# Kernel tuning notes

Hardware: AMD Instinct MI355X
Metric: run time of the kernel (lower is better)

Reference implementation:

```python
import jax, jax.numpy as jnp
import numpy as np

T, B, I, H = 512, 64, 1024, 1024
G = 4 * H + 1  # 4 LSTM gates + 1 boundary gate (HM-LSTM)
STDV = 1.0 / np.sqrt(H)


def setup_inputs() -> dict:
    key = jax.random.key(0)
    ks = jax.random.split(key, 5)
    u = lambda k, shape: jax.random.uniform(k, shape, jnp.float32, -STDV, STDV)
    return {
        "x": jax.random.normal(ks[0], (T, B, I), jnp.float32),
        "W_ih": u(ks[1], (G, I)),
        "W_hh": u(ks[2], (G, H)),
        "b_ih": u(ks[3], (G,)),
        "b_hh": u(ks[4], (G,)),
    }


def reference(x, W_ih, W_hh, b_ih, b_hh):
    h_dim = W_hh.shape[1]
    # Precompute input contribution for all timesteps in one big GEMM: [T,B,G]
    gx_all = jnp.einsum("tbi,gi->tbg", x, W_ih) + b_ih + b_hh
    Bsz = x.shape[1]
    h0 = jnp.zeros((Bsz, h_dim), x.dtype)
    c0 = jnp.zeros((Bsz, h_dim), x.dtype)

    def step(carry, gx):
        h, c = carry
        g = gx + h @ W_hh.T  # [B, 4H+1]
        i = jax.nn.sigmoid(g[:, :h_dim])
        f = jax.nn.sigmoid(g[:, h_dim:2 * h_dim])
        gg = jnp.tanh(g[:, 2 * h_dim:3 * h_dim])
        o = jax.nn.sigmoid(g[:, 3 * h_dim:4 * h_dim])
        z = jax.nn.sigmoid(g[:, 4 * h_dim:])  # [B,1] boundary gate
        ig = i * gg
        # HM-LSTM soft boundary: FLUSH (c=i*g) when z->1, UPDATE otherwise
        c_new = z * ig + (1.0 - z) * (f * c + ig)
        h_new = o * jnp.tanh(c_new)
        return (h_new, c_new), h_new

    (hT, cT), out = jax.lax.scan(step, (h0, c0), gx_all)
    return out, hT, cT
```

## Files before the change

### kernel.cpp

```cpp
#include <hip/hip_runtime.h>
#include <cstdint>
#include <cstddef>

typedef unsigned short u16;
typedef short bf16x8 __attribute__((ext_vector_type(8)));
typedef u16   u16x8  __attribute__((ext_vector_type(8)));
typedef float f32x4  __attribute__((ext_vector_type(4)));

#define NT  512
#define NB  64
#define NH  1024
#define NTB 32768
#define G4  4096

#define AS1C(p) ((const __attribute__((address_space(1))) void*)(p))
#define AS3(p)  ((__attribute__((address_space(3))) void*)(p))

__device__ __forceinline__ float b2f(u16 u){
  return __uint_as_float(((unsigned)u) << 16);
}
__device__ __forceinline__ u16 f2b(float f){
  unsigned u = __float_as_uint(f);
  return (u16)((u + 0x7fffu + ((u >> 16) & 1u)) >> 16);
}
__device__ __forceinline__ float fsigmoid(float x){
  return __builtin_amdgcn_rcpf(1.f + __builtin_amdgcn_exp2f(-1.442695041f * x));
}
__device__ __forceinline__ float ftanh(float x){
  return 2.f * __builtin_amdgcn_rcpf(1.f + __builtin_amdgcn_exp2f(-2.885390082f * x)) - 1.f;
}

__global__ void cvt_bf16(const float* __restrict__ in, u16* __restrict__ out, int n8){
  int stride = gridDim.x * blockDim.x;
  for (int i = blockIdx.x * blockDim.x + threadIdx.x; i < n8; i += stride){
    const float4* p = (const float4*)(in + (size_t)i * 8);
    float4 a = p[0], b = p[1];
    u16x8 r;
    r[0]=f2b(a.x); r[1]=f2b(a.y); r[2]=f2b(a.z); r[3]=f2b(a.w);
    r[4]=f2b(b.x); r[5]=f2b(b.y); r[6]=f2b(b.z); r[7]=f2b(b.w);
    *(u16x8*)(out + (size_t)i * 8) = r;
  }
}

__global__ void zpre_kernel(const float* __restrict__ x, const float* __restrict__ Wih,
                            const float* __restrict__ b_ih, const float* __restrict__ b_hh,
                            float* __restrict__ zp){
  int gw   = (blockIdx.x * 256 + threadIdx.x) >> 6;
  int lane = threadIdx.x & 63;
  const float* wz = Wih + (size_t)4096 * 1024;
  float4 wv[4];
  #pragma unroll
  for (int j = 0; j < 4; ++j) wv[j] = *(const float4*)&wz[lane*16 + j*4];
  float bz = b_ih[4096] + b_hh[4096];
  for (int r = gw; r < NTB; r += 1024){
    const float* xr = x + (size_t)r * 1024 + lane * 16;
    float s = 0.f;
    #pragma unroll
    for (int j = 0; j < 4; ++j){
      float4 xv = *(const float4*)&xr[j*4];
      s += xv.x*wv[j].x + xv.y*wv[j].y + xv.z*wv[j].z + xv.w*wv[j].w;
    }
    #pragma unroll
    for (int o = 32; o > 0; o >>= 1) s += __shfl_down(s, o);
    if (lane == 0) zp[r] = s + bz;
  }
}

template<typename GT>
__global__ __launch_bounds__(256, 2) void gemm_gx(
    const u16* __restrict__ Xb, const u16* __restrict__ Wb,
    const float* __restrict__ b_ih, const float* __restrict__ b_hh,
    GT* __restrict__ gx)
{
  __shared__ u16 As[128*32];
  __shared__ u16 Bs[128*32];
  const int tid  = threadIdx.x;
  const int lane = tid & 63, wave = tid >> 6;
  const int wr = wave >> 1, wc = wave & 1;
  const int m0 = (blockIdx.x & 255) * 128;
  const int n0 = (blockIdx.x >> 8) * 128;
  const int srow = wave * 16 + (lane >> 2);
  const int scol = (lane & 3) * 8;
  const u16* gA = Xb + (size_t)(m0 + srow) * 1024 + scol;
  const u16* gB = Wb + (size_t)(n0 + srow) * 1024 + scol;
  char* lA = (char*)As + wave * 1024;
  char* lB = (char*)Bs + wave * 1024;
  const int fr = lane & 15, fo = (lane >> 4) * 8;

  f32x4 acc[4][4] = {};
  for (int k0 = 0; k0 < 1024; k0 += 32){
    __syncthreads();
    __builtin_amdgcn_global_load_lds(AS1C(gA + k0),            AS3(lA),        16, 0, 0);
    __builtin_amdgcn_global_load_lds(AS1C(gA + 64*1024 + k0),  AS3(lA + 4096), 16, 0, 0);
    __builtin_amdgcn_global_load_lds(AS1C(gB + k0),            AS3(lB),        16, 0, 0);
    __builtin_amdgcn_global_load_lds(AS1C(gB + 64*1024 + k0),  AS3(lB + 4096), 16, 0, 0);
    __syncthreads();
    bf16x8 a[4], b[4];
    #pragma unroll
    for (int mi = 0; mi < 4; ++mi)
      a[mi] = *(const bf16x8*)&As[(wr*64 + mi*16 + fr)*32 + fo];
    #pragma unroll
    for (int ni = 0; ni < 4; ++ni)
      b[ni] = *(const bf16x8*)&Bs[(wc*64 + ni*16 + fr)*32 + fo];
    #pragma unroll
    for (int mi = 0; mi < 4; ++mi)
      #pragma unroll
      for (int ni = 0; ni < 4; ++ni)
        acc[mi][ni] = __builtin_amdgcn_mfma_f32_16x16x32_bf16(a[mi], b[ni], acc[mi][ni], 0, 0, 0);
  }
  const int orow = (lane >> 4) * 4, ocol = lane & 15;
  #pragma unroll
  for (int ni = 0; ni < 4; ++ni){
    const int g = n0 + wc*64 + ni*16 + ocol;
    const float bias = b_ih[g] + b_hh[g];
    #pragma unroll
    for (int mi = 0; mi < 4; ++mi){
      const size_t rb = (size_t)(m0 + wr*64 + mi*16 + orow);
      #pragma unroll
      for (int r = 0; r < 4; ++r){
        float v = acc[mi][ni][r] + bias;
        if constexpr (sizeof(GT) == 4)
          __builtin_nontemporal_store(v, (float*)gx + (rb + r)*G4 + g);
        else
          __builtin_nontemporal_store(f2b(v), (u16*)gx + (rb + r)*G4 + g);
      }
    }
  }
}

__device__ __forceinline__ uint4 ld_h(const uint4* p, bool fb){
  uint4 r;
  if (fb) asm volatile("global_load_dwordx4 %0, %1, off sc0 sc1" : "=v"(r) : "v"(p) : "memory");
  else    asm volatile("global_load_dwordx4 %0, %1, off sc0"     : "=v"(r) : "v"(p) : "memory");
  return r;
}

template<typename GT>
__global__ __launch_bounds__(512, 2) void hmlstm_scan(
    const u16* __restrict__ Whhb, const float* __restrict__ Whhf,
    const GT* __restrict__ gx, const float* __restrict__ zpre,
    unsigned* __restrict__ hdw, float* __restrict__ out)
{
  const int tid  = threadIdx.x;
  const int lane = tid & 63, wave = tid >> 6;
  const int gw = wave >> 1, cb = wave & 1;
  const int fr = lane & 15, hi4 = lane >> 4;
  const int g  = blockIdx.x & 7;
  const int hb = blockIdx.x >> 3;

  __shared__ u16   hs[8*1024];
  __shared__ float wzf[1024];
  __shared__ float glds[4][8][32];
  __shared__ float zsum[8];

  for (int i = tid; i < 1024; i += 512) wzf[i] = Whhf[(size_t)4096*1024 + i];

  const int grow = gw*1024 + hb*32 + cb*16 + fr;
  bf16x8 Bw[32];
  #pragma unroll
  for (int kc = 0; kc < 32; ++kc)
    Bw[kc] = *(const bf16x8*)&Whhb[(size_t)grow*1024 + kc*32 + hi4*8];
  #pragma unroll
  for (int kc = 0; kc < 32; ++kc)
    asm volatile("" : "+v"(Bw[kc]));

  if (tid < 256){
    int b = tid >> 5, c = tid & 31;
    unsigned* p = hdw + (size_t)(g*8 + b)*1024 + hb*32 + c;
    unsigned v0 = 1u;
    asm volatile("global_store_dword %0, %1, off sc0 sc1" :: "v"(p), "v"(v0) : "memory");
  }

  const int srow = wave;
  const int scol = (lane) * 16;
  float c_reg = 0.f;
  bool  fb = false;

  for (int t = 0; t < NT; ++t){
    const unsigned* src = hdw + (size_t)(t & 1) * 65536;
    unsigned*       dst = hdw + (size_t)((t + 1) & 1) * 65536;
    const unsigned  tgt = (unsigned)(t + 1);
    const unsigned* rbase = src + (size_t)(g*8 + srow)*1024 + scol;

    uint4 v[4];
    #pragma unroll
    for (int q = 0; q < 4; ++q) v[q] = ld_h((const uint4*)(rbase + q*4), fb);

    float gxl[4]; float zpc;
    {
      const GT* gp = gx + ((size_t)t*64 + g*8 + (hi4 & 1)*4)*G4 + grow;
      if constexpr (sizeof(GT) == 4){
        #pragma unroll
        for (int r = 0; r < 4; ++r)
          asm volatile("global_load_dword %0, %1, off nt" : "=v"(gxl[r]) : "v"((const float*)gp + (size_t)r*G4) : "memory");
      } else {
        #pragma unroll
        for (int r = 0; r < 4; ++r)
          asm volatile("global_load_ushort %0, %1, off nt" : "=v"(*(unsigned*)&gxl[r]) : "v"((const u16*)gp + (size_t)r*G4) : "memory");
      }
      asm volatile("global_load_dword %0, %1, off" : "=v"(zpc) : "v"(zpre + t*64 + g*8 + ((tid>>5)&7)) : "memory");
    }
    asm volatile("s_waitcnt vmcnt(5)" ::: "memory");
    __builtin_amdgcn_sched_barrier(0);

    unsigned pend = 0;
    #pragma unroll
    for (int q = 0; q < 4; ++q){
      unsigned m = ((v[q].x^tgt)|(v[q].y^tgt)|(v[q].z^tgt)|(v[q].w^tgt)) & 0xFFFFu;
      pend |= (m == 0) ? 0u : (1u << q);
    }
    int spin = 0;
    while (__any((int)(pend != 0u))){
      if (++spin > 8){ fb = true; }
      fb = (bool)__any((int)fb);
      #pragma unroll
      for (int q = 0; q < 4; ++q)
        if (__any((int)((pend >> q) & 1u)))
          v[q] = ld_h((const uint4*)(rbase + q*4), fb);
      asm volatile("s_waitcnt vmcnt(0)" ::: "memory");
      __builtin_amdgcn_sched_barrier(0);
      #pragma unroll
      for (int q = 0; q < 4; ++q){
        if ((pend >> q) & 1u){
          unsigned m = ((v[q].x^tgt)|(v[q].y^tgt)|(v[q].z^tgt)|(v[q].w^tgt)) & 0xFFFFu;
          if (m == 0) pend &= ~(1u << q);
        }
      }
    }

    #pragma unroll
    for (int q = 0; q < 4; ++q){
      unsigned p0 = (v[q].x >> 16) | (v[q].y & 0xFFFF0000u);
      unsigned p1 = (v[q].z >> 16) | (v[q].w & 0xFFFF0000u);
      uint2 pw = {p0, p1};
      int u16b = lane*32 + (q >> 1)*16;
      int addr = srow*2048 + ((u16b ^ (srow << 4))) + (q & 1)*8;
      *(uint2*)((char*)hs + addr) = pw;
    }
    __syncthreads();

    f32x4 acc0 = {}, acc1 = {}, acc2 = {}, acc3 = {};
    const int arow = fr & 7;
    #pragma unroll
    for (int kc = 0; kc < 32; kc += 4){
      bf16x8 a0 = *(const bf16x8*)((char*)hs + arow*2048 + (((kc+0)*64 + hi4*16) ^ (arow << 4)));
      bf16x8 a1 = *(const bf16x8*)((char*)hs + arow*2048 + (((kc+1)*64 + hi4*16) ^ (arow << 4)));
      bf16x8 a2 = *(const bf16x8*)((char*)hs + arow*2048 + (((kc+2)*64 + hi4*16) ^ (arow << 4)));
      bf16x8 a3 = *(const bf16x8*)((char*)hs + arow*2048 + (((kc+3)*64 + hi4*16) ^ (arow << 4)));
      acc0 = __builtin_amdgcn_mfma_f32_16x16x32_bf16(a0, Bw[kc+0], acc0, 0, 0, 0);
      acc1 = __builtin_amdgcn_mfma_f32_16x16x32_bf16(a1, Bw[kc+1], acc1, 0, 0, 0);
      acc2 = __builtin_amdgcn_mfma_f32_16x16x32_bf16(a2, Bw[kc+2], acc2, 0, 0, 0);
      acc3 = __builtin_amdgcn_mfma_f32_16x16x32_bf16(a3, Bw[kc+3], acc3, 0, 0, 0);
    }
    f32x4 ac = (acc0 + acc1) + (acc2 + acc3);

    {
      int bz = wave;
      float zp = 0.f;
      int b0 = bz*2048 + ((lane*32) ^ (bz << 4));
      int b1 = bz*2048 + ((lane*32 + 16) ^ (bz << 4));
      bf16x8 h0 = *(const bf16x8*)((char*)hs + b0);
      bf16x8 h1 = *(const bf16x8*)((char*)hs + b1);
      #pragma unroll
      for (int e = 0; e < 8; ++e){
        zp += b2f((u16)h0[e]) * wzf[lane*16 + e];
        zp += b2f((u16)h1[e]) * wzf[lane*16 + 8 + e];
      }
      #pragma unroll
      for (int o = 32; o > 0; o >>= 1) zp += __shfl_xor(zp, o);
      if (lane == 0) zsum[bz] = zp;
    }

    asm volatile("s_waitcnt vmcnt(0)" ::: "memory");
    __builtin_amdgcn_sched_barrier(0);

    if constexpr (sizeof(GT) != 4){
      #pragma unroll
      for (int r = 0; r < 4; ++r)
        gxl[r] = __uint_as_float((*(unsigned*)&gxl[r]) << 16);
    }

    if (hi4 < 2){
      #pragma unroll
      for (int r = 0; r < 4; ++r){
        float vv = ac[r] + gxl[r];
        float s = (gw == 2) ? ftanh(vv) : fsigmoid(vv);
        glds[gw][hi4*4 + r][cb*16 + fr] = s;
      }
    }
    __syncthreads();

    if (tid < 256){
      int b = tid >> 5, c = tid & 31;
      float iv  = glds[0][b][c], fvg = glds[1][b][c];
      float gv  = glds[2][b][c], ov  = glds[3][b][c];
      float zv  = fsigmoid(zpc + zsum[b]);
      float ig  = iv * gv;
      float cn  = zv*ig + (1.f - zv)*(fvg*c_reg + ig);
      float hv_ = ov * ftanh(cn);
      c_reg = cn;
      const int hoff = (g*8 + b)*1024 + hb*32 + c;
      unsigned pv = ((unsigned)f2b(hv_) << 16) | (unsigned)(t + 2);
      asm volatile("global_store_dword %0, %1, off sc0 sc1" :: "v"(dst + hoff), "v"(pv) : "memory");
      __builtin_nontemporal_store(hv_, out + (size_t)t*65536 + hoff);
      if (t == NT-1){
        out[(size_t)NT*65536 + hoff] = hv_;
        out[(size_t)NT*65536 + 65536 + hoff] = cn;
      }
    }
  }
}

extern "C" void kernel_launch(void* const* d_in, const int* in_sizes, int n_in,
                              void* d_out, int out_size, void* d_ws, size_t ws_size,
                              hipStream_t stream)
{
  (void)in_sizes; (void)n_in; (void)out_size;
  const float* x    = (const float*)d_in[0];
  const float* Wih  = (const float*)d_in[1];
  const float* Whh  = (const float*)d_in[2];
  const float* b_ih = (const float*)d_in[3];
  const float* b_hh = (const float*)d_in[4];
  float* out = (float*)d_out;

  size_t off = 0;
  auto alloc = [&](size_t bytes)->void*{
    void* p = (char*)d_ws + off;
    off = (off + bytes + 255) & ~(size_t)255;
    return p;
  };
  u16*  xb    = (u16*) alloc((size_t)NTB*1024*2);
  u16*  wihb  = (u16*) alloc((size_t)4097*1024*2);
  u16*  whhb  = (u16*) alloc((size_t)4097*1024*2);
  unsigned* hdw = (unsigned*)alloc((size_t)2*65536*4);
  float* zp   = (float*)alloc((size_t)NTB*4);
  bool g32 = (ws_size >= off + (size_t)NTB*G4*4);
  void* gxp = (char*)d_ws + off;

  hipMemsetAsync(hdw, 0, (size_t)2*65536*4, stream);
  cvt_bf16<<<dim3(2048), dim3(256), 0, stream>>>(x,   xb,   NTB*1024/8);
  cvt_bf16<<<dim3(512),  dim3(256), 0, stream>>>(Wih, wihb, 4097*1024/8);
  cvt_bf16<<<dim3(512),  dim3(256), 0, stream>>>(Whh, whhb, 4097*1024/8);
  zpre_kernel<<<dim3(256), dim3(256), 0, stream>>>(x, Wih, b_ih, b_hh, zp);
  if (g32){
    float* gxf = (float*)gxp;
    gemm_gx<float><<<dim3(8192), dim3(256), 0, stream>>>(xb, wihb, b_ih, b_hh, gxf);
    void* args[] = { (void*)&whhb, (void*)&Whh, (void*)&gxf, (void*)&zp, (void*)&hdw, (void*)&out };
    if (hipLaunchCooperativeKernel((void*)hmlstm_scan<float>, dim3(256), dim3(512),
                                   args, 0, stream) != hipSuccess)
      hmlstm_scan<float><<<dim3(256), dim3(512), 0, stream>>>(whhb, Whh, gxf, zp, hdw, out);
  } else {
    u16* gxb = (u16*)gxp;
    gemm_gx<u16><<<dim3(8192), dim3(256), 0, stream>>>(xb, wihb, b_ih, b_hh, gxb);
    void* args[] = { (void*)&whhb, (void*)&Whh, (void*)&gxb, (void*)&zp, (void*)&hdw, (void*)&out };
    if (hipLaunchCooperativeKernel((void*)hmlstm_scan<u16>, dim3(256), dim3(512),
                                   args, 0, stream) != hipSuccess)
      hmlstm_scan<u16><<<dim3(256), dim3(512), 0, stream>>>(whhb, Whh, gxb, zp, hdw, out);
  }
}
```

Before: 3.577 ms.

## Keep W_hh fragments in AGPRs and fuse boundary-gate dot into h unpack

```diff
diff --git a/kernel.cpp b/kernel.cpp
--- a/kernel.cpp
+++ b/kernel.cpp
@@ -137,9 +137,9 @@
 
 template<typename GT>
 __global__ __launch_bounds__(512, 2) void hmlstm_scan(
-    const u16* __restrict__ Whhb, const float* __restrict__ Whhf,
-    const GT* __restrict__ gx, const float* __restrict__ zpre,
-    unsigned* __restrict__ hdw, float* __restrict__ out)
+    const u16* __restrict__ Whhb, const GT* __restrict__ gx,
+    const float* __restrict__ zpre, unsigned* __restrict__ hdw,
+    float* __restrict__ out)
 {
   const int tid  = threadIdx.x;
   const int lane = tid & 63, wave = tid >> 6;
@@ -149,12 +149,9 @@
   const int hb = blockIdx.x >> 3;
 
   __shared__ u16   hs[8*1024];
-  __shared__ float wzf[1024];
   __shared__ float glds[4][8][32];
   __shared__ float zsum[8];
 
-  for (int i = tid; i < 1024; i += 512) wzf[i] = Whhf[(size_t)4096*1024 + i];
-
   const int grow = gw*1024 + hb*32 + cb*16 + fr;
   bf16x8 Bw[32];
   #pragma unroll
@@ -162,7 +159,12 @@
     Bw[kc] = *(const bf16x8*)&Whhb[(size_t)grow*1024 + kc*32 + hi4*8];
   #pragma unroll
   for (int kc = 0; kc < 32; ++kc)
-    asm volatile("" : "+v"(Bw[kc]));
+    asm volatile("" : "+a"(Bw[kc]));
+
+  uint2 wzr[4];
+  #pragma unroll
+  for (int q = 0; q < 4; ++q)
+    wzr[q] = *(const uint2*)&Whhb[(size_t)4096*1024 + lane*16 + q*4];
 
   if (tid < 256){
     int b = tid >> 5, c = tid & 31;
@@ -172,7 +174,7 @@
   }
 
   const int srow = wave;
-  const int scol = (lane) * 16;
+  const int scol = lane * 16;
   float c_reg = 0.f;
   bool  fb = false;
 
@@ -228,15 +230,23 @@
       }
     }
 
+    float zp = 0.f;
     #pragma unroll
     for (int q = 0; q < 4; ++q){
       unsigned p0 = (v[q].x >> 16) | (v[q].y & 0xFFFF0000u);
       unsigned p1 = (v[q].z >> 16) | (v[q].w & 0xFFFF0000u);
+      zp = fmaf(__uint_as_float(p0 << 16),         __uint_as_float(wzr[q].x << 16),         zp);
+      zp = fmaf(__uint_as_float(p0 & 0xFFFF0000u), __uint_as_float(wzr[q].x & 0xFFFF0000u), zp);
+      zp = fmaf(__uint_as_float(p1 << 16),         __uint_as_float(wzr[q].y << 16),         zp);
+      zp = fmaf(__uint_as_float(p1 & 0xFFFF0000u), __uint_as_float(wzr[q].y & 0xFFFF0000u), zp);
       uint2 pw = {p0, p1};
       int u16b = lane*32 + (q >> 1)*16;
       int addr = srow*2048 + ((u16b ^ (srow << 4))) + (q & 1)*8;
       *(uint2*)((char*)hs + addr) = pw;
     }
+    #pragma unroll
+    for (int o = 32; o > 0; o >>= 1) zp += __shfl_xor(zp, o);
+    if (lane == 0) zsum[srow] = zp;
     __syncthreads();
 
     f32x4 acc0 = {}, acc1 = {}, acc2 = {}, acc3 = {};
@@ -247,29 +257,13 @@
       bf16x8 a1 = *(const bf16x8*)((char*)hs + arow*2048 + (((kc+1)*64 + hi4*16) ^ (arow << 4)));
       bf16x8 a2 = *(const bf16x8*)((char*)hs + arow*2048 + (((kc+2)*64 + hi4*16) ^ (arow << 4)));
       bf16x8 a3 = *(const bf16x8*)((char*)hs + arow*2048 + (((kc+3)*64 + hi4*16) ^ (arow << 4)));
-      acc0 = __builtin_amdgcn_mfma_f32_16x16x32_bf16(a0, Bw[kc+0], acc0, 0, 0, 0);
-      acc1 = __builtin_amdgcn_mfma_f32_16x16x32_bf16(a1, Bw[kc+1], acc1, 0, 0, 0);
-      acc2 = __builtin_amdgcn_mfma_f32_16x16x32_bf16(a2, Bw[kc+2], acc2, 0, 0, 0);
-      acc3 = __builtin_amdgcn_mfma_f32_16x16x32_bf16(a3, Bw[kc+3], acc3, 0, 0, 0);
-    }
+      asm volatile("v_mfma_f32_16x16x32_bf16 %0, %1, %2, %0" : "+v"(acc0) : "v"(a0), "a"(Bw[kc+0]));
+      asm volatile("v_mfma_f32_16x16x32_bf16 %0, %1, %2, %0" : "+v"(acc1) : "v"(a1), "a"(Bw[kc+1]));
+      asm volatile("v_mfma_f32_16x16x32_bf16 %0, %1, %2, %0" : "+v"(acc2) : "v"(a2), "a"(Bw[kc+2]));
+      asm volatile("v_mfma_f32_16x16x32_bf16 %0, %1, %2, %0" : "+v"(acc3) : "v"(a3), "a"(Bw[kc+3]));
+    }
+    asm volatile("s_nop 7\n\ts_nop 7\n\ts_nop 7" :::);
     f32x4 ac = (acc0 + acc1) + (acc2 + acc3);
-
-    {
-      int bz = wave;
-      float zp = 0.f;
-      int b0 = bz*2048 + ((lane*32) ^ (bz << 4));
-      int b1 = bz*2048 + ((lane*32 + 16) ^ (bz << 4));
-      bf16x8 h0 = *(const bf16x8*)((char*)hs + b0);
-      bf16x8 h1 = *(const bf16x8*)((char*)hs + b1);
-      #pragma unroll
-      for (int e = 0; e < 8; ++e){
-        zp += b2f((u16)h0[e]) * wzf[lane*16 + e];
-        zp += b2f((u16)h1[e]) * wzf[lane*16 + 8 + e];
-      }
-      #pragma unroll
-      for (int o = 32; o > 0; o >>= 1) zp += __shfl_xor(zp, o);
-      if (lane == 0) zsum[bz] = zp;
-    }
 
     asm volatile("s_waitcnt vmcnt(0)" ::: "memory");
     __builtin_amdgcn_sched_barrier(0);
@@ -345,16 +339,16 @@
   if (g32){
     float* gxf = (float*)gxp;
     gemm_gx<float><<<dim3(8192), dim3(256), 0, stream>>>(xb, wihb, b_ih, b_hh, gxf);
-    void* args[] = { (void*)&whhb, (void*)&Whh, (void*)&gxf, (void*)&zp, (void*)&hdw, (void*)&out };
+    void* args[] = { (void*)&whhb, (void*)&gxf, (void*)&zp, (void*)&hdw, (void*)&out };
     if (hipLaunchCooperativeKernel((void*)hmlstm_scan<float>, dim3(256), dim3(512),
                                    args, 0, stream) != hipSuccess)
-      hmlstm_scan<float><<<dim3(256), dim3(512), 0, stream>>>(whhb, Whh, gxf, zp, hdw, out);
+      hmlstm_scan<float><<<dim3(256), dim3(512), 0, stream>>>(whhb, gxf, zp, hdw, out);
   } else {
     u16* gxb = (u16*)gxp;
     gemm_gx<u16><<<dim3(8192), dim3(256), 0, stream>>>(xb, wihb, b_ih, b_hh, gxb);
-    void* args[] = { (void*)&whhb, (void*)&Whh, (void*)&gxb, (void*)&zp, (void*)&hdw, (void*)&out };
+    void* args[] = { (void*)&whhb, (void*)&gxb, (void*)&zp, (void*)&hdw, (void*)&out };
     if (hipLaunchCooperativeKernel((void*)hmlstm_scan<u16>, dim3(256), dim3(512),
                                    args, 0, stream) != hipSuccess)
-      hmlstm_scan<u16><<<dim3(256), dim3(512), 0, stream>>>(whhb, Whh, gxb, zp, hdw, out);
-  }
-}
+      hmlstm_scan<u16><<<dim3(256), dim3(512), 0, stream>>>(whhb, gxb, zp, hdw, out);
+  }
+}
```

New measurement: 3.457 ms. -3.4%, faster.
